# Performance work log

Measured on AMD Instinct MI355X. Metric: run time of the kernel, lower is better.

The kernel has to match this reference:

```python
import jax, jax.numpy as jnp
import numpy as np

HEAD_K_DIM = 128  # linear_key_head_dim (not derivable from weight shapes alone)
EPS_NORM = 1e-6


def _l2norm(x, eps=1e-6):
    return x * jax.lax.rsqrt(jnp.sum(x * x, axis=-1, keepdims=True) + eps)


def setup_inputs() -> dict:
    key = jax.random.key(0)
    ks = jax.random.split(key, 9)
    B, S, H = 2, 1024, 2048
    Hv, Hk, Dk, Dv, K = 32, 16, 128, 128, 4
    key_dim, value_dim = Hk * Dk, Hv * Dv
    C = 2 * key_dim + value_dim  # conv_dim = 8192
    s = 0.02
    return {
        "hidden_states": jax.random.normal(ks[0], (B, S, H), jnp.float32),
        "conv_state": jnp.zeros((B, C, K - 1), jnp.float32),
        "recurrent_state": jnp.zeros((B, Hv, Dk, Dv), jnp.float32),
        "W_qkv": (jax.random.normal(ks[1], (C, H)) * s).astype(jnp.float32),
        "W_z": (jax.random.normal(ks[2], (value_dim, H)) * s).astype(jnp.float32),
        "W_b": (jax.random.normal(ks[3], (Hv, H)) * s).astype(jnp.float32),
        "W_a": (jax.random.normal(ks[4], (Hv, H)) * s).astype(jnp.float32),
        "conv_w": (jax.random.normal(ks[5], (C, K)) * s).astype(jnp.float32),
        "dt_bias": jnp.ones((Hv,), jnp.float32),
        "A_log": jnp.log(jax.random.uniform(ks[6], (Hv,), jnp.float32, 1e-3, 16.0)),
        "norm_weight": jnp.ones((Dv,), jnp.float32),
        "W_out": (jax.random.normal(ks[7], (H, value_dim)) * s).astype(jnp.float32),
    }


def reference(hidden_states, conv_state, recurrent_state, W_qkv, W_z, W_b, W_a,
              conv_w, dt_bias, A_log, norm_weight, W_out):
    B, S, H = hidden_states.shape
    Hv = dt_bias.shape[0]
    Dv = norm_weight.shape[0]
    C, K = conv_w.shape
    value_dim = Hv * Dv
    key_dim = (C - value_dim) // 2
    Dk = HEAD_K_DIM
    Hk = key_dim // Dk

    # input projections
    mixed_qkv = jnp.einsum('bsh,ch->bcs', hidden_states, W_qkv)  # (B, C, S)
    z = hidden_states @ W_z.T                                    # (B, S, value_dim)
    b = hidden_states @ W_b.T                                    # (B, S, Hv)
    a = hidden_states @ W_a.T                                    # (B, S, Hv)

    # causal depthwise conv over time with cached prefix state
    padded = jnp.concatenate([conv_state, mixed_qkv], axis=-1)   # (B, C, K-1+S)
    conv_out = sum(padded[:, :, k:k + S] * conv_w[:, k][None, :, None]
                   for k in range(K))                            # (B, C, S)
    conv_state_new = padded[:, :, -(K - 1):]
    mixed = jnp.swapaxes(jax.nn.silu(conv_out), 1, 2)            # (B, S, C)

    q = mixed[..., :key_dim].reshape(B, S, Hk, Dk)
    k = mixed[..., key_dim:2 * key_dim].reshape(B, S, Hk, Dk)
    v = mixed[..., 2 * key_dim:].reshape(B, S, Hv, Dv)

    beta = jax.nn.sigmoid(b)                                     # (B, S, Hv)
    g = -jnp.exp(A_log) * jax.nn.softplus(a + dt_bias)           # (B, S, Hv)

    rep = Hv // Hk
    if rep > 1:
        q = jnp.repeat(q, rep, axis=2)
        k = jnp.repeat(k, rep, axis=2)

    scale = Dk ** (-0.5)
    q = _l2norm(q) * scale
    k = _l2norm(k)

    # time-leading for scan: (S, B, Hv, ...)
    qT, kT, vT = (jnp.moveaxis(x, 1, 0) for x in (q, k, v))
    gT, betaT = jnp.moveaxis(g, 1, 0), jnp.moveaxis(beta, 1, 0)

    def step(state, xs):
        q_t, k_t, v_t, g_t, beta_t = xs
        state = state * jnp.exp(g_t)[..., None, None]            # decay
        kv_mem = jnp.einsum('bhk,bhkv->bhv', k_t, state)         # read
        delta = (v_t - kv_mem) * beta_t[..., None]               # correction
        state = state + jnp.einsum('bhk,bhv->bhkv', k_t, delta)  # write
        out_t = jnp.einsum('bhk,bhkv->bhv', q_t, state)          # readout
        return state, out_t

    final_state, outs = jax.lax.scan(step, recurrent_state.astype(jnp.float32),
                                     (qT, kT, vT, gT, betaT))
    core = jnp.moveaxis(outs, 0, 1)                              # (B, S, Hv, Dv)

    # gated RMS norm per value head
    var = jnp.mean(core * core, axis=-1, keepdims=True)
    xn = core * jax.lax.rsqrt(var + EPS_NORM) * norm_weight
    gated = xn * jax.nn.silu(z.reshape(B, S, Hv, Dv))

    output = gated.reshape(B, S, value_dim) @ W_out.T            # (B, S, H)
    return output, conv_state_new, final_state
```

## Files before the change

kernel.cpp:

```cpp
#include <hip/hip_runtime.h>
#include <cstdint>
#include <cstddef>

#define B_ 2
#define S_ 1024
#define H_ 2048
#define HV_ 32
#define HK_ 16
#define DK_ 128
#define DV_ 128
#define CC_ 8192
#define KEYDIM_ 2048
#define VALDIM_ 4096
#define NC_ 16
#define CS_ 64
#define NBIG 12416
#define NBIGP 12544

typedef __attribute__((ext_vector_type(8))) short bf16x8;
typedef __attribute__((ext_vector_type(4))) float f32x4;

__device__ __forceinline__ ushort f2bf_rne(float x) {
  union { float f; uint32_t u; } c; c.f = x;
  uint32_t u = c.u + 0x7FFFu + ((c.u >> 16) & 1u);
  return (ushort)(u >> 16);
}

__device__ __forceinline__ void gld16(const void* g, void* l) {
  __builtin_amdgcn_global_load_lds(
      (const __attribute__((address_space(1))) void*)g,
      (__attribute__((address_space(3))) void*)l, 16, 0, 0);
}

__global__ void f2bf_kernel(const float* __restrict__ in, ushort* __restrict__ out, int n) {
  int i = (blockIdx.x * 256 + threadIdx.x) * 4;
  if (i >= n) return;
  float4 v = *(const float4*)(in + i);
  ushort4 o;
  o.x = f2bf_rne(v.x); o.y = f2bf_rne(v.y);
  o.z = f2bf_rne(v.z); o.w = f2bf_rne(v.w);
  *(ushort4*)(out + i) = o;
}

__global__ void wcat_kernel(const float* __restrict__ Wqkv, const float* __restrict__ Wz,
                            const float* __restrict__ Wb, const float* __restrict__ Wa,
                            ushort* __restrict__ out) {
  int i = (blockIdx.x * 256 + threadIdx.x) * 4;
  if (i >= NBIGP * H_) return;
  int n = i >> 11;
  int k = i & (H_ - 1);
  float4 v = make_float4(0.f, 0.f, 0.f, 0.f);
  if (n < 8192)       v = *(const float4*)(Wqkv + (size_t)n * H_ + k);
  else if (n < 12288) v = *(const float4*)(Wz + (size_t)(n - 8192) * H_ + k);
  else if (n < 12320) v = *(const float4*)(Wb + (size_t)(n - 12288) * H_ + k);
  else if (n < 12352) v = *(const float4*)(Wa + (size_t)(n - 12320) * H_ + k);
  ushort4 o;
  o.x = f2bf_rne(v.x); o.y = f2bf_rne(v.y);
  o.z = f2bf_rne(v.z); o.w = f2bf_rne(v.w);
  *(ushort4*)(out + i) = o;
}

#define MEMF() asm volatile("" ::: "memory")
#define VMW(n) asm volatile("s_waitcnt vmcnt(" #n ")" ::: "memory")
#define LGKM(n) asm volatile("s_waitcnt lgkmcnt(" #n ")" ::: "memory")
#define BARR() do { __builtin_amdgcn_s_barrier(); MEMF(); } while (0)

__global__ __launch_bounds__(512, 2) void gemm256_8ph(
    const ushort* __restrict__ A, const ushort* __restrict__ B,
    float* __restrict__ C, int Ns, int K)
{
  __shared__ ushort sAm[2][16384];
  __shared__ ushort sBm[2][16384];

  const int t = threadIdx.x;
  const int wave = t >> 6, lane = t & 63;
  const int wm = wave >> 2, wn = wave & 3;
  const int l15 = lane & 15, l4 = lane >> 4;
  const int mt = blockIdx.x, nt = blockIdx.y;

  const int rgS0 = (wave & 3) + (wave >> 2) * 8;
  const int rgS3 = rgS0 + 4;
  const int rgS1 = (wave & 1) + (wave >> 1) * 4;
  const int rgS2 = rgS1 + 2;

  const ushort* aP0 = A + (size_t)(mt * 256 + rgS0 * 16 + l15) * K + l4 * 8;
  const ushort* aP1 = A + (size_t)(mt * 256 + rgS3 * 16 + l15) * K + l4 * 8;
  const ushort* bP0 = B + (size_t)(nt * 256 + rgS1 * 16 + l15) * K + l4 * 8;
  const ushort* bP1 = B + (size_t)(nt * 256 + rgS2 * 16 + l15) * K + l4 * 8;

  f32x4 acc[8][4];
  #pragma unroll
  for (int i = 0; i < 8; i++)
    #pragma unroll
    for (int j = 0; j < 4; j++)
      #pragma unroll
      for (int r = 0; r < 4; r++) acc[i][j][r] = 0.f;

  bf16x8 aF[8], bF[4];

  gld16(aP0,      &sAm[0][(rgS0 * 2 + 0) * 512]);
  gld16(aP1,      &sAm[0][(rgS3 * 2 + 0) * 512]);
  gld16(bP0,      &sBm[0][(rgS1 * 2 + 0) * 512]);
  gld16(bP1,      &sBm[0][(rgS2 * 2 + 0) * 512]);
  MEMF();
  gld16(aP0 + 32, &sAm[0][(rgS0 * 2 + 1) * 512]);
  gld16(aP1 + 32, &sAm[0][(rgS3 * 2 + 1) * 512]);
  gld16(bP0 + 32, &sBm[0][(rgS1 * 2 + 1) * 512]);
  gld16(bP1 + 32, &sBm[0][(rgS2 * 2 + 1) * 512]);
  MEMF();
  VMW(4); BARR();

  const int NT = K >> 6;
  for (int tt = 0; tt < NT; tt++) {
    const int c = tt & 1, o = c ^ 1;
    const int kq = (tt + 1 < NT) ? (tt + 1) << 6 : 0;
    #pragma unroll
    for (int h = 0; h < 2; h++) {
      #pragma unroll
      for (int i = 0; i < 8; i++)
        aF[i] = *(const bf16x8*)(&sAm[c][((wm * 8 + i) * 2 + h) * 512 + lane * 8]);
      #pragma unroll
      for (int j = 0; j < 4; j++)
        bF[j] = *(const bf16x8*)(&sBm[c][((wn * 4 + j) * 2 + h) * 512 + lane * 8]);
      MEMF();
      gld16(aP0 + kq + h * 32, &sAm[o][(rgS0 * 2 + h) * 512]);
      gld16(aP1 + kq + h * 32, &sAm[o][(rgS3 * 2 + h) * 512]);
      gld16(bP0 + kq + h * 32, &sBm[o][(rgS1 * 2 + h) * 512]);
      gld16(bP1 + kq + h * 32, &sBm[o][(rgS2 * 2 + h) * 512]);
      MEMF();
      LGKM(8);
      BARR();
      LGKM(0);
      __builtin_amdgcn_sched_barrier(0);
      __builtin_amdgcn_s_setprio(1);
      #pragma unroll
      for (int i = 0; i < 8; i++)
        #pragma unroll
        for (int j = 0; j < 4; j++)
          acc[i][j] = __builtin_amdgcn_mfma_f32_16x16x32_bf16(aF[i], bF[j], acc[i][j], 0, 0, 0);
      __builtin_amdgcn_s_setprio(0);
      VMW(4);
      BARR();
    }
  }
  VMW(0);

  #pragma unroll
  for (int mf = 0; mf < 8; mf++) {
    const int row0 = mt * 256 + wm * 128 + mf * 16 + l4 * 4;
    #pragma unroll
    for (int nf = 0; nf < 4; nf++) {
      const int col = nt * 256 + wn * 64 + nf * 16 + l15;
      if (col < Ns) {
        #pragma unroll
        for (int r = 0; r < 4; r++)
          C[(size_t)(row0 + r) * Ns + col] = acc[mf][nf][r];
      }
    }
  }
}

__device__ __forceinline__ void stage_tile(
    const ushort* aS0, const ushort* aS1, const ushort* bS0, const ushort* bS1,
    ushort* ldsA, ushort* ldsB, int wave, int k0)
{
  #pragma unroll
  for (int h = 0; h < 2; h++) {
    gld16(aS0 + k0 + h * 32, ldsA + h * 4096 + (wave * 2 + 0) * 512);
    gld16(aS1 + k0 + h * 32, ldsA + h * 4096 + (wave * 2 + 1) * 512);
    gld16(bS0 + k0 + h * 32, ldsB + h * 4096 + (wave * 2 + 0) * 512);
    gld16(bS1 + k0 + h * 32, ldsB + h * 4096 + (wave * 2 + 1) * 512);
  }
}

__global__ __launch_bounds__(256) void gemm_bf16_nt(
    const ushort* __restrict__ A, const ushort* __restrict__ B,
    float* __restrict__ C, int M, int N, int K)
{
  __shared__ ushort sL[2][2][8192];
  int t = threadIdx.x;
  int wave = t >> 6, lane = t & 63;
  int wm = wave >> 1, wn = wave & 1;
  int lrow = lane & 15, quad = lane >> 4;
  int mt = blockIdx.x, nt = blockIdx.y;

  f32x4 acc[4][4];
  #pragma unroll
  for (int i = 0; i < 4; i++)
    #pragma unroll
    for (int j = 0; j < 4; j++)
      #pragma unroll
      for (int r = 0; r < 4; r++) acc[i][j][r] = 0.f;

  const ushort* aS0 = A + (size_t)(mt * 128 + (wave * 2 + 0) * 16 + lrow) * K + quad * 8;
  const ushort* aS1 = A + (size_t)(mt * 128 + (wave * 2 + 1) * 16 + lrow) * K + quad * 8;
  const ushort* bS0 = B + (size_t)(nt * 128 + (wave * 2 + 0) * 16 + lrow) * K + quad * 8;
  const ushort* bS1 = B + (size_t)(nt * 128 + (wave * 2 + 1) * 16 + lrow) * K + quad * 8;

  stage_tile(aS0, aS1, bS0, bS1, &sL[0][0][0], &sL[0][1][0], wave, 0);
  __syncthreads();

  const int NK = K >> 6;
  for (int it = 0; it < NK; it++) {
    if (it + 1 < NK)
      stage_tile(aS0, aS1, bS0, bS1,
                 &sL[(it + 1) & 1][0][0], &sL[(it + 1) & 1][1][0],
                 wave, (it + 1) * 64);
    const ushort* bufA = &sL[it & 1][0][0];
    const ushort* bufB = &sL[it & 1][1][0];
    #pragma unroll
    for (int h = 0; h < 2; h++) {
      bf16x8 af[4], bfr[4];
      #pragma unroll
      for (int i = 0; i < 4; i++)
        af[i] = *(const bf16x8*)(bufA + h * 4096 + (wm * 4 + i) * 512 + lane * 8);
      #pragma unroll
      for (int j = 0; j < 4; j++)
        bfr[j] = *(const bf16x8*)(bufB + h * 4096 + (wn * 4 + j) * 512 + lane * 8);
      #pragma unroll
      for (int i = 0; i < 4; i++)
        #pragma unroll
        for (int j = 0; j < 4; j++)
          acc[i][j] = __builtin_amdgcn_mfma_f32_16x16x32_bf16(af[i], bfr[j], acc[i][j], 0, 0, 0);
    }
    __syncthreads();
  }

  #pragma unroll
  for (int i = 0; i < 4; i++) {
    int m_base = mt * 128 + wm * 64 + i * 16 + quad * 4;
    #pragma unroll
    for (int j = 0; j < 4; j++) {
      int n = nt * 128 + wn * 64 + j * 16 + lrow;
      #pragma unroll
      for (int rr = 0; rr < 4; rr++)
        C[(size_t)(m_base + rr) * N + n] = acc[i][j][rr];
    }
  }
}

__global__ void convstate_kernel(const float* __restrict__ Cbig,
                                 float* __restrict__ out)
{
  int idx = blockIdx.x * blockDim.x + threadIdx.x;
  if (idx >= B_ * CC_ * 3) return;
  int j = idx % 3;
  int c = (idx / 3) % CC_;
  int b = idx / (3 * CC_);
  out[idx] = Cbig[((size_t)(b * S_ + (S_ - 3 + j))) * NBIG + c];
}

__global__ __launch_bounds__(128) void prep_qkv(
    const float* __restrict__ Cbig, const float* __restrict__ conv_state,
    const float* __restrict__ conv_w,
    float* __restrict__ Qn, float* __restrict__ Kn, float* __restrict__ Vb)
{
  int group = blockIdx.x, s = blockIdx.y, b = blockIdx.z;
  int t = threadIdx.x;
  int c = group * 128 + t;
  float acc = 0.f;
  #pragma unroll
  for (int kk = 0; kk < 4; kk++) {
    int sp = s - 3 + kk;
    float x = (sp < 0) ? conv_state[((size_t)(b * CC_ + c)) * 3 + (3 + sp)]
                       : Cbig[((size_t)(b * S_ + sp)) * NBIG + c];
    acc += conv_w[c * 4 + kk] * x;
  }
  float val = acc / (1.f + __expf(-acc));

  if (group < 32) {
    __shared__ float red2[2];
    float p = val * val;
    #pragma unroll
    for (int off = 32; off > 0; off >>= 1) p += __shfl_xor(p, off);
    if ((t & 63) == 0) red2[t >> 6] = p;
    __syncthreads();
    float r = rsqrtf(red2[0] + red2[1] + 1e-6f);
    if (group < 16) {
      r *= 0.08838834764831845f;
      Qn[(((size_t)(b * HK_ + group)) * S_ + s) * DK_ + t] = val * r;
    } else {
      Kn[(((size_t)(b * HK_ + (group - 16))) * S_ + s) * DK_ + t] = val * r;
    }
  } else {
    Vb[(((size_t)(b * HV_ + (group - 32))) * S_ + s) * DV_ + t] = val;
  }
}

__global__ void prep_gb(const float* __restrict__ Cbig,
                        const float* __restrict__ A_log, const float* __restrict__ dt_bias,
                        float* __restrict__ g_buf, float* __restrict__ beta_buf)
{
  int idx = blockIdx.x * blockDim.x + threadIdx.x;
  if (idx >= B_ * HV_ * S_) return;
  int s = idx & (S_ - 1);
  int hv = (idx >> 10) & 31;
  int b = idx >> 15;
  float bv = Cbig[((size_t)(b * S_ + s)) * NBIG + 12288 + hv];
  float av = Cbig[((size_t)(b * S_ + s)) * NBIG + 12320 + hv];
  float x = av + dt_bias[hv];
  float sp = (x > 20.f) ? x : log1pf(__expf(x));
  g_buf[idx] = -__expf(A_log[hv]) * sp;
  beta_buf[idx] = 1.f / (1.f + __expf(-bv));
}

__device__ __forceinline__ int swf4(int r, int f) { return r * 32 + (f ^ (r & 31)); }

__global__ __launch_bounds__(256) void cp_kernel(
    const float* __restrict__ Qn, const float* __restrict__ Kn,
    const float* __restrict__ Vb,
    const float* __restrict__ g_buf, const float* __restrict__ beta_buf,
    float* __restrict__ G_buf, float* __restrict__ M_buf,
    float* __restrict__ KcD, float* __restrict__ D0p)
{
  __shared__ float sK[64 * 128];
  __shared__ float sX[32 * 128];
  __shared__ float sT[64 * 65];
  __shared__ float sGB[128];
  float* sG  = sGB;
  float* sBe = sGB + 64;
  float* sA  = sX;
  float* tTw = sX;
  float* tTb = sX;
  float4* sK4 = (float4*)sK;
  float4* sX4 = (float4*)sX;

  const int ch = blockIdx.x;
  const int bh = ch / NC_, c = ch % NC_;
  const int b = bh >> 5, hv = bh & 31, hk = hv >> 1;
  const int s0 = c * CS_;
  const int t = threadIdx.x;
  const size_t gOff = (size_t)bh * S_ + s0;

  if (t < 64) {
    float Gw0 = g_buf[gOff + t];
    #pragma unroll
    for (int off = 1; off < 64; off <<= 1) {
      float o = __shfl_up(Gw0, off);
      if (t >= off) Gw0 += o;
    }
    G_buf[gOff + t] = Gw0;
    sG[t] = Gw0;
    sBe[t] = beta_buf[gOff + t];
  }
  {
    const float4* src = (const float4*)(Kn + ((size_t)(b * HK_ + hk) * S_ + s0) * DK_);
    #pragma unroll
    for (int u = 0; u < 8; u++) {
      int idx = u * 256 + t;
      sK4[swf4(idx >> 5, idx & 31)] = src[idx];
    }
  }
  __syncthreads();

  const float4* qsrc = (const float4*)(Qn + ((size_t)(b * HK_ + hk) * S_ + s0) * DK_);
  {
    int ti2 = t >> 4, tj = t & 15;
    for (int h = 0; h < 2; h++) {
      #pragma unroll
      for (int u = 0; u < 4; u++) {
        int idx = u * 256 + t;
        sX4[swf4(idx >> 5, idx & 31)] = qsrc[h * 1024 + idx];
      }
      __syncthreads();
      float accM[2][4];
      #pragma unroll
      for (int a = 0; a < 2; a++)
        #pragma unroll
        for (int e = 0; e < 4; e++) accM[a][e] = 0.f;
      for (int k4 = 0; k4 < 32; k4++) {
        float4 qv[2], kv[4];
        qv[0] = sX4[swf4(ti2, k4)];
        qv[1] = sX4[swf4(ti2 + 16, k4)];
        #pragma unroll
        for (int e = 0; e < 4; e++) kv[e] = sK4[swf4(tj + 16 * e, k4)];
        #pragma unroll
        for (int a = 0; a < 2; a++)
          #pragma unroll
          for (int e = 0; e < 4; e++)
            accM[a][e] += qv[a].x * kv[e].x + qv[a].y * kv[e].y +
                          qv[a].z * kv[e].z + qv[a].w * kv[e].w;
      }
      #pragma unroll
      for (int a = 0; a < 2; a++) {
        int iG = h * 32 + ti2 + 16 * a;
        float Gi = sG[iG];
        #pragma unroll
        for (int e = 0; e < 4; e++) {
          int j = tj + 16 * e;
          float m = (j <= iG) ? __expf(Gi - sG[j]) * accM[a][e] : 0.f;
          M_buf[(size_t)ch * 4096 + iG * 64 + j] = m;
        }
      }
      __syncthreads();
    }
  }

  {
    int ti = t >> 4, tj = t & 15;
    float accA[4][4];
    #pragma unroll
    for (int a = 0; a < 4; a++)
      #pragma unroll
      for (int e = 0; e < 4; e++) accA[a][e] = 0.f;
    for (int k4 = 0; k4 < 32; k4++) {
      float4 ki[4], kj[4];
      #pragma unroll
      for (int e = 0; e < 4; e++) {
        ki[e] = sK4[swf4(ti + 16 * e, k4)];
        kj[e] = sK4[swf4(tj + 16 * e, k4)];
      }
      #pragma unroll
      for (int a = 0; a < 4; a++)
        #pragma unroll
        for (int e = 0; e < 4; e++)
          accA[a][e] += ki[a].x * kj[e].x + ki[a].y * kj[e].y +
                        ki[a].z * kj[e].z + ki[a].w * kj[e].w;
    }
    float resA[4][4];
    #pragma unroll
    for (int a = 0; a < 4; a++) {
      int i = ti + 16 * a;
      float Gi = sG[i], Bi = sBe[i];
      #pragma unroll
      for (int e = 0; e < 4; e++) {
        int j = tj + 16 * e;
        resA[a][e] = (j < i) ? Bi * __expf(Gi - sG[j]) * accA[a][e] : 0.f;
      }
    }
    __syncthreads();
    #pragma unroll
    for (int a = 0; a < 4; a++)
      #pragma unroll
      for (int e = 0; e < 4; e++)
        sA[(ti + 16 * a) * 64 + (tj + 16 * e)] = resA[a][e];
  }
  __syncthreads();

  if (t < 64) {
    sT[t] = (t == 0) ? 1.f : 0.f;
    for (int i = 1; i < 64; i++) {
      float acc = 0.f;
      for (int j = 0; j < i; j++) acc += sA[i * 64 + j] * sT[j * 65 + t];
      sT[i * 65 + t] = ((t == i) ? 1.f : 0.f) - acc;
    }
  }
  __syncthreads();

  #pragma unroll
  for (int u = 0; u < 16; u++) {
    int idx = u * 256 + t;
    int tcol = idx & 63;
    int j = idx >> 6;
    float wj = sBe[j] * __expf(sG[j]);
    tTw[j * 64 + tcol] = sT[tcol * 65 + j] * wj;
  }
  __syncthreads();

  {
    int i04 = t >> 4, tk = t & 15;
    float accK[4][8];
    #pragma unroll
    for (int r = 0; r < 4; r++)
      #pragma unroll
      for (int u = 0; u < 8; u++) accK[r][u] = 0.f;
    for (int j = 0; j < 64; j++) {
      float4 tw = ((float4*)tTw)[j * 16 + i04];
      float4 ka = sK4[swf4(j, tk * 2)];
      float4 kb = sK4[swf4(j, tk * 2 + 1)];
      float tws[4] = {tw.x, tw.y, tw.z, tw.w};
      float kvv[8] = {ka.x, ka.y, ka.z, ka.w, kb.x, kb.y, kb.z, kb.w};
      #pragma unroll
      for (int r = 0; r < 4; r++)
        #pragma unroll
        for (int u = 0; u < 8; u++)
          accK[r][u] += tws[r] * kvv[u];
    }
    size_t base = (size_t)ch * NBIG;
    #pragma unroll
    for (int r = 0; r < 4; r++) {
      *(float4*)(&KcD[base + (size_t)(i04 * 4 + r) * 128 + tk * 8]) =
          make_float4(accK[r][0], accK[r][1], accK[r][2], accK[r][3]);
      *(float4*)(&KcD[base + (size_t)(i04 * 4 + r) * 128 + tk * 8 + 4]) =
          make_float4(accK[r][4], accK[r][5], accK[r][6], accK[r][7]);
    }
  }
  __syncthreads();

  #pragma unroll
  for (int u = 0; u < 16; u++) {
    int idx = u * 256 + t;
    int tcol = idx & 63;
    int j = idx >> 6;
    tTb[j * 64 + tcol] = sT[tcol * 65 + j] * sBe[j];
  }
  {
    const float4* src = (const float4*)(Vb + ((size_t)bh * S_ + s0) * DV_);
    #pragma unroll
    for (int u = 0; u < 8; u++) {
      int idx = u * 256 + t;
      sK4[swf4(idx >> 5, idx & 31)] = src[idx];
    }
  }
  __syncthreads();

  {
    int i04 = t >> 4, tv_ = t & 15;
    float accD[4][8];
    #pragma unroll
    for (int r = 0; r < 4; r++)
      #pragma unroll
      for (int u = 0; u < 8; u++) accD[r][u] = 0.f;
    for (int j = 0; j < 64; j++) {
      float4 tb = ((float4*)tTb)[j * 16 + i04];
      float4 va = sK4[swf4(j, tv_ * 2)];
      float4 vb = sK4[swf4(j, tv_ * 2 + 1)];
      float tbs[4] = {tb.x, tb.y, tb.z, tb.w};
      float vvv[8] = {va.x, va.y, va.z, va.w, vb.x, vb.y, vb.z, vb.w};
      #pragma unroll
      for (int r = 0; r < 4; r++)
        #pragma unroll
        for (int u = 0; u < 8; u++)
          accD[r][u] += tbs[r] * vvv[u];
    }
    size_t base = (size_t)ch * NBIG;
    #pragma unroll
    for (int r = 0; r < 4; r++) {
      *(float4*)(&D0p[base + (size_t)(i04 * 4 + r) * 128 + tv_ * 8]) =
          make_float4(accD[r][0], accD[r][1], accD[r][2], accD[r][3]);
      *(float4*)(&D0p[base + (size_t)(i04 * 4 + r) * 128 + tv_ * 8 + 4]) =
          make_float4(accD[r][4], accD[r][5], accD[r][6], accD[r][7]);
    }
  }
}

__global__ __launch_bounds__(512) void phaseb_kernel(
    const float* __restrict__ rec_state, const float* __restrict__ Qn,
    const float* __restrict__ Kn, const float* __restrict__ G_buf,
    float* __restrict__ KcD, const float* __restrict__ D0p,
    float* __restrict__ Oq_buf, float* __restrict__ final_state)
{
  __shared__ float sS[128 * 32];
  __shared__ float sKT[128 * 64];
  __shared__ float sQT[128 * 64];
  __shared__ float sD[64 * 32];
  __shared__ float sR[2][64 * 32];

  const int blk = blockIdx.x;
  const int bh = (blk & 7) | ((blk >> 5) << 3);
  const int vq = (blk >> 3) & 3;
  const int b = bh >> 5, hv = bh & 31, hk = hv >> 1;
  const int t = threadIdx.x;
  const int vbase = vq * 32;
  const float* gG = G_buf + (size_t)bh * S_;

  #pragma unroll
  for (int u = 0; u < 2; u++) {
    int idx = u * 512 + t;
    int k = idx >> 3;
    int v4 = (idx & 7) * 4;
    *(float4*)(&sS[k * 32 + v4]) =
        *(const float4*)(&rec_state[((size_t)bh * 128 + k) * 128 + vbase + v4]);
  }
  __syncthreads();

  const int si = t & 63, skq = t >> 6;
  const int kg = t >> 8;
  const int tt = t & 255;
  const int ti = tt >> 3, tv = t & 7;
  const int tp = t >> 3;

  for (int c = 0; c < NC_; c++) {
    const size_t ch = (size_t)bh * NC_ + c;
    const int s0 = c * CS_;
    const float GC = gG[s0 + 63];
    const float eGC = __expf(GC);

    {
      float eGi = __expf(gG[s0 + si]);
      const float* kcRow = KcD + ch * NBIG + si * 128 + skq * 16;
      const float* qRow  = Qn + ((size_t)(b * HK_ + hk) * S_ + s0 + si) * DK_ + skq * 16;
      #pragma unroll
      for (int u = 0; u < 4; u++) {
        float4 kc = *(const float4*)(kcRow + u * 4);
        float4 qv = *(const float4*)(qRow + u * 4);
        int kk = skq * 16 + u * 4;
        sKT[(kk + 0) * 64 + si] = kc.x; sKT[(kk + 1) * 64 + si] = kc.y;
        sKT[(kk + 2) * 64 + si] = kc.z; sKT[(kk + 3) * 64 + si] = kc.w;
        sQT[(kk + 0) * 64 + si] = qv.x * eGi; sQT[(kk + 1) * 64 + si] = qv.y * eGi;
        sQT[(kk + 2) * 64 + si] = qv.z * eGi; sQT[(kk + 3) * 64 + si] = qv.w * eGi;
      }
    }
    __syncthreads();

    {
      float accD[2][4], accO[2][4];
      #pragma unroll
      for (int r = 0; r < 2; r++) {
        accO[r][0] = accO[r][1] = accO[r][2] = accO[r][3] = 0.f;
        accD[r][0] = accD[r][1] = accD[r][2] = accD[r][3] = 0.f;
      }
      if (kg == 0) {
        #pragma unroll
        for (int r = 0; r < 2; r++) {
          float4 d0 = *(const float4*)(&D0p[ch * NBIG + (size_t)(ti * 2 + r) * 128 + vbase + tv * 4]);
          accD[r][0] = d0.x; accD[r][1] = d0.y; accD[r][2] = d0.z; accD[r][3] = d0.w;
        }
      }
      const int k0 = kg << 6;
      for (int k = k0; k < k0 + 64; k++) {
        float2 kc = *(const float2*)(&sKT[k * 64 + ti * 2]);
        float2 qb = *(const float2*)(&sQT[k * 64 + ti * 2]);
        float4 sv = *(const float4*)(&sS[k * 32 + tv * 4]);
        accD[0][0] -= kc.x * sv.x; accD[0][1] -= kc.x * sv.y;
        accD[0][2] -= kc.x * sv.z; accD[0][3] -= kc.x * sv.w;
        accD[1][0] -= kc.y * sv.x; accD[1][1] -= kc.y * sv.y;
        accD[1][2] -= kc.y * sv.z; accD[1][3] -= kc.y * sv.w;
        accO[0][0] += qb.x * sv.x; accO[0][1] += qb.x * sv.y;
        accO[0][2] += qb.x * sv.z; accO[0][3] += qb.x * sv.w;
        accO[1][0] += qb.y * sv.x; accO[1][1] += qb.y * sv.y;
        accO[1][2] += qb.y * sv.z; accO[1][3] += qb.y * sv.w;
      }
      if (kg == 1) {
        #pragma unroll
        for (int r = 0; r < 2; r++) {
          int i = ti * 2 + r;
          *(float4*)(&sR[0][i * 32 + tv * 4]) =
              make_float4(accD[r][0], accD[r][1], accD[r][2], accD[r][3]);
          *(float4*)(&sR[1][i * 32 + tv * 4]) =
              make_float4(accO[r][0], accO[r][1], accO[r][2], accO[r][3]);
        }
      }
      __syncthreads();
      if (kg == 0) {
        #pragma unroll
        for (int r = 0; r < 2; r++) {
          int i = ti * 2 + r;
          float4 pD = *(const float4*)(&sR[0][i * 32 + tv * 4]);
          float4 pO = *(const float4*)(&sR[1][i * 32 + tv * 4]);
          float4 dv = make_float4(accD[r][0] + pD.x, accD[r][1] + pD.y,
                                  accD[r][2] + pD.z, accD[r][3] + pD.w);
          float4 ov = make_float4(accO[r][0] + pO.x, accO[r][1] + pO.y,
                                  accO[r][2] + pO.z, accO[r][3] + pO.w);
          *(float4*)(&sD[i * 32 + tv * 4]) = dv;
          *(float4*)(&KcD[ch * NBIG + (size_t)i * 128 + vbase + tv * 4]) = dv;
          *(float4*)(&Oq_buf[ch * 8192 + (size_t)i * 128 + vbase + tv * 4]) = ov;
        }
      }
    }

    {
      float sc = __expf(GC - gG[s0 + si]);
      const float* kRow = Kn + ((size_t)(b * HK_ + hk) * S_ + s0 + si) * DK_ + skq * 16;
      #pragma unroll
      for (int u = 0; u < 4; u++) {
        float4 x = *(const float4*)(kRow + u * 4);
        x.x *= sc; x.y *= sc; x.z *= sc; x.w *= sc;
        int kgr = skq * 4 + u;
        *(float4*)(&sKT[si * 128 + 4 * (kgr ^ (si & 31))]) = x;
      }
    }
    __syncthreads();

    {
      float acc[2][4];
      acc[0][0] = acc[0][1] = acc[0][2] = acc[0][3] = 0.f;
      acc[1][0] = acc[1][1] = acc[1][2] = acc[1][3] = 0.f;
      const int kgr = tp >> 1, kh = (tp & 1) * 2;
      for (int i = 0; i < 64; i++) {
        float4 d  = *(const float4*)(&sD[i * 32 + tv * 4]);
        float2 ka = *(const float2*)(&sKT[i * 128 + 4 * (kgr ^ (i & 31)) + kh]);
        acc[0][0] += ka.x * d.x; acc[0][1] += ka.x * d.y;
        acc[0][2] += ka.x * d.z; acc[0][3] += ka.x * d.w;
        acc[1][0] += ka.y * d.x; acc[1][1] += ka.y * d.y;
        acc[1][2] += ka.y * d.z; acc[1][3] += ka.y * d.w;
      }
      #pragma unroll
      for (int r = 0; r < 2; r++) {
        int k = tp * 2 + r;
        float4 s = *(const float4*)(&sS[k * 32 + tv * 4]);
        s.x = s.x * eGC + acc[r][0]; s.y = s.y * eGC + acc[r][1];
        s.z = s.z * eGC + acc[r][2]; s.w = s.w * eGC + acc[r][3];
        *(float4*)(&sS[k * 32 + tv * 4]) = s;
      }
    }
    __syncthreads();
  }

  #pragma unroll
  for (int u = 0; u < 2; u++) {
    int idx = u * 512 + t;
    int k = idx >> 3;
    int v4 = (idx & 7) * 4;
    *(float4*)(&final_state[((size_t)bh * 128 + k) * 128 + vbase + v4]) =
        *(const float4*)(&sS[k * 32 + v4]);
  }
}

__global__ __launch_bounds__(128) void phasec_kernel(
    const float* __restrict__ KcD, const float* __restrict__ Oq_buf,
    const float* __restrict__ M_buf, const float* __restrict__ norm_weight,
    const float* __restrict__ Cbig, ushort* __restrict__ zg_bf)
{
  __shared__ float sM[4096];
  __shared__ float red[2][2];
  int ch = blockIdx.x;
  int bh = ch / NC_, c = ch % NC_;
  int b = bh >> 5, hv = bh & 31;
  int s0 = c * CS_;
  int v = threadIdx.x;

  float Dr[64];
  #pragma unroll
  for (int j = 0; j < 64; j++) Dr[j] = KcD[(size_t)ch * NBIG + j * 128 + v];
  {
    const float4* src = (const float4*)(M_buf + (size_t)ch * 4096);
    #pragma unroll
    for (int u = 0; u < 8; u++) ((float4*)sM)[u * 128 + v] = src[u * 128 + v];
  }
  __syncthreads();
  float nw = norm_weight[v];

  for (int i = 0; i < 64; i++) {
    float o = Oq_buf[(size_t)ch * 8192 + i * 128 + v];
    const float4* mr = (const float4*)(sM + i * 64);
    #pragma unroll
    for (int j4 = 0; j4 < 16; j4++) {
      float4 m = mr[j4];
      o += m.x * Dr[4 * j4] + m.y * Dr[4 * j4 + 1] +
           m.z * Dr[4 * j4 + 2] + m.w * Dr[4 * j4 + 3];
    }
    float p = o * o;
    #pragma unroll
    for (int off = 32; off > 0; off >>= 1) p += __shfl_xor(p, off);
    if ((v & 63) == 0) red[i & 1][v >> 6] = p;
    __syncthreads();
    float var = (red[i & 1][0] + red[i & 1][1]) * (1.f / 128.f);
    float xn = o * rsqrtf(var + 1e-6f) * nw;
    float zv = Cbig[((size_t)(b * S_ + s0 + i)) * NBIG + 8192 + hv * DV_ + v];
    zg_bf[((size_t)(b * S_ + s0 + i)) * VALDIM_ + hv * DV_ + v] =
        f2bf_rne(xn * (zv / (1.f + __expf(-zv))));
  }
}

extern "C" void kernel_launch(void* const* d_in, const int* in_sizes, int n_in,
                              void* d_out, int out_size, void* d_ws, size_t ws_size,
                              hipStream_t stream)
{
  const float* hs          = (const float*)d_in[0];
  const float* conv_state  = (const float*)d_in[1];
  const float* rec_state   = (const float*)d_in[2];
  const float* W_qkv       = (const float*)d_in[3];
  const float* W_z         = (const float*)d_in[4];
  const float* W_b         = (const float*)d_in[5];
  const float* W_a         = (const float*)d_in[6];
  const float* conv_w      = (const float*)d_in[7];
  const float* dt_bias     = (const float*)d_in[8];
  const float* A_log       = (const float*)d_in[9];
  const float* norm_weight = (const float*)d_in[10];
  const float* W_out       = (const float*)d_in[11];

  float* out       = (float*)d_out;
  float* out_conv  = out + (size_t)B_ * S_ * H_;
  float* out_state = out_conv + (size_t)B_ * CC_ * 3;

  float* ws = (float*)d_ws;
  float* Cbig = ws;
  float* KcD  = Cbig;
  float* D0p  = Cbig + (size_t)1024 * NBIG;
  float* g_buf    = ws + 25427968;
  float* beta_buf = ws + 25493504;
  float* G_buf    = ws + 25559040;
  float* Qn       = ws + 25624576;
  float* Kn       = ws + 29818880;
  float* Vb       = ws + 34013184;
  float* M_buf    = ws + 42401792;
  float* Oq_buf   = Vb;

  ushort* Wcat_bf = (ushort*)(ws + 25427968);
  ushort* hs_bf   = (ushort*)(ws + 38273024);
  ushort* zg_bf   = (ushort*)Qn;
  ushort* Wout_bf = (ushort*)Kn;

  const int M = B_ * S_;

  f2bf_kernel<<<(M * H_) / 1024, 256, 0, stream>>>(hs, hs_bf, M * H_);
  wcat_kernel<<<(NBIGP * H_) / 1024, 256, 0, stream>>>(W_qkv, W_z, W_b, W_a, Wcat_bf);
  gemm256_8ph<<<dim3(M / 256, NBIGP / 256), 512, 0, stream>>>(hs_bf, Wcat_bf, Cbig, NBIG, H_);
  convstate_kernel<<<(B_ * CC_ * 3 + 255) / 256, 256, 0, stream>>>(Cbig, out_conv);
  prep_qkv<<<dim3(64, S_, B_), 128, 0, stream>>>(Cbig, conv_state, conv_w, Qn, Kn, Vb);
  prep_gb<<<(B_ * HV_ * S_ + 255) / 256, 256, 0, stream>>>(Cbig, A_log, dt_bias, g_buf, beta_buf);
  cp_kernel<<<B_ * HV_ * NC_, 256, 0, stream>>>(Qn, Kn, Vb, g_buf, beta_buf,
                                                G_buf, M_buf, KcD, D0p);
  phaseb_kernel<<<B_ * HV_ * 4, 512, 0, stream>>>(rec_state, Qn, Kn, G_buf,
                                                  KcD, D0p, Oq_buf, out_state);
  f2bf_kernel<<<(H_ * VALDIM_) / 1024, 256, 0, stream>>>(W_out, Wout_bf, H_ * VALDIM_);
  phasec_kernel<<<B_ * HV_ * NC_, 128, 0, stream>>>(KcD, Oq_buf, M_buf,
                                                    norm_weight, Cbig, zg_bf);
  gemm_bf16_nt<<<dim3(M / 128, H_ / 128), 256, 0, stream>>>(zg_bf, Wout_bf, out, M, H_, VALDIM_);
}
```

Baseline: 863.2 us.

## Prefetch next chunk's K, Q, Kc and D0 into registers in phase B

Software-pipelines the sequential chunk loop of the recurrent phase-B kernel. The next chunk's Kc, Q, K and D0 rows are loaded into registers while the current chunk computes, so global-load latency leaves the serial critical path. The gate vector is staged once into shared memory, and the inner loops are unrolled by four. This adds register pressure and extra loads on the last chunk, which may lower occupancy.

```diff
diff --git a/kernel.cpp b/kernel.cpp
--- a/kernel.cpp
+++ b/kernel.cpp
@@ -545,6 +545,7 @@
   __shared__ float sQT[128 * 64];
   __shared__ float sD[64 * 32];
   __shared__ float sR[2][64 * 32];
+  __shared__ float sGf[1024];
 
   const int blk = blockIdx.x;
   const int bh = (blk & 7) | ((blk >> 5) << 3);
@@ -562,6 +563,8 @@
     *(float4*)(&sS[k * 32 + v4]) =
         *(const float4*)(&rec_state[((size_t)bh * 128 + k) * 128 + vbase + v4]);
   }
+  sGf[t] = gG[t];
+  sGf[t + 512] = gG[t + 512];
   __syncthreads();
 
   const int si = t & 63, skq = t >> 6;
@@ -570,20 +573,41 @@
   const int ti = tt >> 3, tv = t & 7;
   const int tp = t >> 3;
 
+  const float* qBase = Qn + ((size_t)(b * HK_ + hk) * S_ + si) * DK_ + skq * 16;
+  const float* kBase = Kn + ((size_t)(b * HK_ + hk) * S_ + si) * DK_ + skq * 16;
+
+  float4 rKc[4], rQ[4], rKn[4], rD0[2];
+  {
+    const size_t ch0 = (size_t)bh * NC_;
+    const float* kcRow = KcD + ch0 * NBIG + si * 128 + skq * 16;
+    #pragma unroll
+    for (int u = 0; u < 4; u++) {
+      rKc[u] = *(const float4*)(kcRow + u * 4);
+      rQ[u]  = *(const float4*)(qBase + u * 4);
+      rKn[u] = *(const float4*)(kBase + u * 4);
+    }
+    if (kg == 0) {
+      #pragma unroll
+      for (int r = 0; r < 2; r++)
+        rD0[r] = *(const float4*)(&D0p[ch0 * NBIG + (size_t)(ti * 2 + r) * 128 + vbase + tv * 4]);
+    }
+  }
+
   for (int c = 0; c < NC_; c++) {
     const size_t ch = (size_t)bh * NC_ + c;
     const int s0 = c * CS_;
-    const float GC = gG[s0 + 63];
+    const int cn = (c + 1 < NC_) ? c + 1 : c;
+    const size_t chn = (size_t)bh * NC_ + cn;
+    const int s0n = cn * CS_;
+    const float GC = sGf[s0 + 63];
     const float eGC = __expf(GC);
 
     {
-      float eGi = __expf(gG[s0 + si]);
-      const float* kcRow = KcD + ch * NBIG + si * 128 + skq * 16;
-      const float* qRow  = Qn + ((size_t)(b * HK_ + hk) * S_ + s0 + si) * DK_ + skq * 16;
+      float eGi = __expf(sGf[s0 + si]);
       #pragma unroll
       for (int u = 0; u < 4; u++) {
-        float4 kc = *(const float4*)(kcRow + u * 4);
-        float4 qv = *(const float4*)(qRow + u * 4);
+        float4 kc = rKc[u];
+        float4 qv = rQ[u];
         int kk = skq * 16 + u * 4;
         sKT[(kk + 0) * 64 + si] = kc.x; sKT[(kk + 1) * 64 + si] = kc.y;
         sKT[(kk + 2) * 64 + si] = kc.z; sKT[(kk + 3) * 64 + si] = kc.w;
@@ -594,6 +618,16 @@
     __syncthreads();
 
     {
+      const float* kcRow = KcD + chn * NBIG + si * 128 + skq * 16;
+      const float* qRow  = qBase + (size_t)s0n * DK_;
+      #pragma unroll
+      for (int u = 0; u < 4; u++) {
+        rKc[u] = *(const float4*)(kcRow + u * 4);
+        rQ[u]  = *(const float4*)(qRow + u * 4);
+      }
+    }
+
+    {
       float accD[2][4], accO[2][4];
       #pragma unroll
       for (int r = 0; r < 2; r++) {
@@ -603,11 +637,12 @@
       if (kg == 0) {
         #pragma unroll
         for (int r = 0; r < 2; r++) {
-          float4 d0 = *(const float4*)(&D0p[ch * NBIG + (size_t)(ti * 2 + r) * 128 + vbase + tv * 4]);
-          accD[r][0] = d0.x; accD[r][1] = d0.y; accD[r][2] = d0.z; accD[r][3] = d0.w;
+          accD[r][0] = rD0[r].x; accD[r][1] = rD0[r].y;
+          accD[r][2] = rD0[r].z; accD[r][3] = rD0[r].w;
         }
       }
       const int k0 = kg << 6;
+      #pragma unroll 4
       for (int k = k0; k < k0 + 64; k++) {
         float2 kc = *(const float2*)(&sKT[k * 64 + ti * 2]);
         float2 qb = *(const float2*)(&sQT[k * 64 + ti * 2]);
@@ -646,19 +681,26 @@
           *(float4*)(&KcD[ch * NBIG + (size_t)i * 128 + vbase + tv * 4]) = dv;
           *(float4*)(&Oq_buf[ch * 8192 + (size_t)i * 128 + vbase + tv * 4]) = ov;
         }
+        #pragma unroll
+        for (int r = 0; r < 2; r++)
+          rD0[r] = *(const float4*)(&D0p[chn * NBIG + (size_t)(ti * 2 + r) * 128 + vbase + tv * 4]);
       }
     }
 
     {
-      float sc = __expf(GC - gG[s0 + si]);
-      const float* kRow = Kn + ((size_t)(b * HK_ + hk) * S_ + s0 + si) * DK_ + skq * 16;
+      float sc = __expf(GC - sGf[s0 + si]);
       #pragma unroll
       for (int u = 0; u < 4; u++) {
-        float4 x = *(const float4*)(kRow + u * 4);
+        float4 x = rKn[u];
         x.x *= sc; x.y *= sc; x.z *= sc; x.w *= sc;
         int kgr = skq * 4 + u;
         *(float4*)(&sKT[si * 128 + 4 * (kgr ^ (si & 31))]) = x;
       }
+    }
+    {
+      const float* kRow = kBase + (size_t)s0n * DK_;
+      #pragma unroll
+      for (int u = 0; u < 4; u++) rKn[u] = *(const float4*)(kRow + u * 4);
     }
     __syncthreads();
 
@@ -667,6 +709,7 @@
       acc[0][0] = acc[0][1] = acc[0][2] = acc[0][3] = 0.f;
       acc[1][0] = acc[1][1] = acc[1][2] = acc[1][3] = 0.f;
       const int kgr = tp >> 1, kh = (tp & 1) * 2;
+      #pragma unroll 4
       for (int i = 0; i < 64; i++) {
         float4 d  = *(const float4*)(&sD[i * 32 + tv * 4]);
         float2 ka = *(const float2*)(&sKT[i * 128 + 4 * (kgr ^ (i & 31)) + kh]);
```

Measured after the change: 836.7 us. 3.1% less time.
